# Kernel optimization log

Measured on AMD Instinct MI355X. Metric: run time of the kernel, lower is better.

The kernel has to match this reference:

```python
import jax, jax.numpy as jnp
import numpy as np

S, IN, OUT = 2048, 512, 512
H, KV = 16, 4            # query heads, kv heads (cross-broadcast + averaged)
DQ = DK = DV = 64        # per-head embedding dims


def setup_inputs() -> dict:
    key = jax.random.key(0)
    ks = jax.random.split(key, 5)
    lim_in = 1.0 / np.sqrt(IN)
    lim_o = 1.0 / np.sqrt(H * DV)
    x = jax.random.normal(ks[0], (S, IN), dtype=jnp.float32)
    Wq = jax.random.uniform(ks[1], (H * DQ, IN), jnp.float32, -lim_in, lim_in)
    Wk = jax.random.uniform(ks[2], (KV * DK, IN), jnp.float32, -lim_in, lim_in)
    Wv = jax.random.uniform(ks[3], (KV * DV, IN), jnp.float32, -lim_in, lim_in)
    Wo = jax.random.uniform(ks[4], (OUT, H * DV), jnp.float32, -lim_o, lim_o)
    return {"x": x, "Wq": Wq, "Wk": Wk, "Wv": Wv, "Wo": Wo}


def reference(x, Wq, Wk, Wv, Wo):
    seq = x.shape[0]
    # projections (eqx.nn.Linear: y = W @ x, no bias)
    q = (x @ Wq.T).reshape(seq, H, DQ)    # [S, H, DQ]
    k = (x @ Wk.T).reshape(seq, KV, DK)   # [S, KV, DK]
    v = (x @ Wv.T).reshape(seq, KV, DV)   # [S, KV, DV]
    # cross-broadcast every kv head against every query head -> [KV, H, S, S]
    scores = jnp.einsum('shd,tkd->khst', q, k) / jnp.sqrt(jnp.asarray(DK, x.dtype))
    # NOTE: original applies causal mask whenever `mask is not None`; the
    # boolean flag is always passed, so masking is effectively always on.
    causal = jnp.tril(jnp.ones((seq, seq), dtype=bool))
    scores = jnp.where(causal, scores, -jnp.inf)
    w = jax.nn.softmax(scores, axis=-1)   # [KV, H, S, S]
    # attn @ V, then sum over kv heads and average by KV
    o = jnp.einsum('khst,tkd->shd', w, v) / KV  # [S, H, DV]
    return o.reshape(seq, H * DV) @ Wo.T        # [S, OUT]
```

## Files before the change

### kernel.cpp

```cpp
#include <hip/hip_runtime.h>
#include <hip/hip_bf16.h>

#define SEQ   2048
#define INF_  512
#define HQ    16
#define KVH   4
#define DH    64
#define NQ    (HQ*DH)
#define NKV   (KVH*DH)
#define OUTD  512

typedef short v8s __attribute__((ext_vector_type(8)));
typedef float v4f __attribute__((ext_vector_type(4)));

static __device__ __forceinline__ float bf2f(unsigned short u) {
    union { unsigned int i; float f; } c;
    c.i = ((unsigned int)u) << 16;
    return c.f;
}
static __device__ __forceinline__ unsigned short f2bf(float f) {
    union { float f; unsigned int i; } c; c.f = f;
    unsigned int lsb = (c.i >> 16) & 1u;
    c.i += 0x7fffu + lsb;
    return (unsigned short)(c.i >> 16);
}
static __device__ __forceinline__ unsigned int f2bf2(float lo, float hi) {
    union { __hip_bfloat162 h; unsigned int u; } c;
    c.h = __float22bfloat162_rn(make_float2(lo, hi));
    return c.u;
}
static __device__ __forceinline__ v8s pack8(v4f a, v4f b) {
    union { v8s s; uint4 u; } c;
    c.u = make_uint4(f2bf2(a[0], a[1]), f2bf2(a[2], a[3]),
                     f2bf2(b[0], b[1]), f2bf2(b[2], b[3]));
    return c.s;
}

static __device__ __forceinline__ void gll16(const void* g, void* l) {
    __builtin_amdgcn_global_load_lds(
        (const __attribute__((address_space(1))) void*)g,
        (__attribute__((address_space(3))) void*)l, 16, 0, 0);
}

static __device__ __forceinline__ void stage_tile(
    const unsigned short* __restrict__ src, int stride, int kb,
    unsigned short* ldsbase, int w, int lane)
{
#pragma unroll
    for (int i = 0; i < 2; i++) {
        const int rl = w * 16 + i * 8 + (lane >> 3);
        const int kc = ((lane & 7) ^ (rl & 7)) * 8;
        gll16(src + (size_t)rl * stride + kb + kc,
              ldsbase + (w * 16 + i * 8) * 64);
    }
}

static __device__ __forceinline__ void stage_tile32(
    const unsigned short* __restrict__ src, int stride, int kb,
    unsigned short* ldsbase, int w, int lane)
{
    const int rl = w * 8 + (lane >> 3);
    const int kc = ((lane & 7) ^ (rl & 7)) * 8;
    gll16(src + (size_t)rl * stride + kb + kc,
          ldsbase + (w * 8) * 64);
}

#define QSCALE 0.180336880f

__global__ __launch_bounds__(256) void cast_all(
    const float* __restrict__ x,  const float* __restrict__ Wq,
    const float* __restrict__ Wk, const float* __restrict__ Wv,
    const float* __restrict__ Wo,
    unsigned short* __restrict__ xb,  unsigned short* __restrict__ Wqb,
    unsigned short* __restrict__ Wkb, unsigned short* __restrict__ Wvb,
    unsigned short* __restrict__ Wob)
{
    size_t i = ((size_t)blockIdx.x * 256 + threadIdx.x) * 8;
    const float* s; unsigned short* d; size_t off;
    if (i < 1048576)      { s = x;  d = xb;  off = i; }
    else if (i < 1572864) { s = Wq; d = Wqb; off = i - 1048576; }
    else if (i < 1703936) { s = Wk; d = Wkb; off = i - 1572864; }
    else if (i < 1835008) { s = Wv; d = Wvb; off = i - 1703936; }
    else                  { s = Wo; d = Wob; off = i - 1835008; }
    float4 a = *(const float4*)(s + off);
    float4 b = *(const float4*)(s + off + 4);
    *(uint4*)(d + off) = make_uint4(f2bf2(a.x, a.y), f2bf2(a.z, a.w),
                                    f2bf2(b.x, b.y), f2bf2(b.z, b.w));
}

__global__ __launch_bounds__(256, 4) void gemm_qkv(
    const unsigned short* __restrict__ xb,
    const unsigned short* __restrict__ Wqb,
    const unsigned short* __restrict__ Wkb,
    const unsigned short* __restrict__ Wvb,
    unsigned short* __restrict__ Qg,
    unsigned short* __restrict__ Kg,
    unsigned short* __restrict__ Vg)
{
    __shared__ unsigned short Asb[2][4096];
    __shared__ unsigned short Bsb[2][4096];

    const int m0 = blockIdx.x * 64;
    const int n0 = blockIdx.y * 64;

    const unsigned short* Bp; int role;
    if (n0 < NQ)            { Bp = Wqb + (size_t)n0 * INF_;              role = 0; }
    else if (n0 < NQ + NKV) { Bp = Wkb + (size_t)(n0 - NQ) * INF_;       role = 1; }
    else                    { Bp = Wvb + (size_t)(n0 - NQ - NKV) * INF_; role = 2; }

    const int tid = threadIdx.x;
    const int w = tid >> 6, lane = tid & 63;
    const int n = lane & 15, quad = lane >> 4;
    const int m7 = n & 7;
    const int r0w = (w & 1) * 32, c0w = (w >> 1) * 32;
    const unsigned short* Ap = xb + (size_t)m0 * INF_;

    v4f acc[2][2];
#pragma unroll
    for (int rt = 0; rt < 2; rt++)
#pragma unroll
        for (int ct = 0; ct < 2; ct++) acc[rt][ct] = (v4f){0.f,0.f,0.f,0.f};

    stage_tile(Ap, INF_, 0, &Asb[0][0], w, lane);
    stage_tile(Bp, INF_, 0, &Bsb[0][0], w, lane);

    for (int kb = 0; kb < INF_; kb += 64) {
        const int buf = (kb >> 6) & 1;
        __syncthreads();
        if (kb + 64 < INF_) {
            stage_tile(Ap, INF_, kb + 64, &Asb[buf ^ 1][0], w, lane);
            stage_tile(Bp, INF_, kb + 64, &Bsb[buf ^ 1][0], w, lane);
        }
#pragma unroll
        for (int kk = 0; kk < 2; kk++) {
            const int gs = ((kk * 4 + quad) ^ m7) * 8;
            v8s a0 = *(const v8s*)&Asb[buf][(r0w + n) * 64 + gs];
            v8s a1 = *(const v8s*)&Asb[buf][(r0w + 16 + n) * 64 + gs];
            v8s b0 = *(const v8s*)&Bsb[buf][(c0w + n) * 64 + gs];
            v8s b1 = *(const v8s*)&Bsb[buf][(c0w + 16 + n) * 64 + gs];
            acc[0][0] = __builtin_amdgcn_mfma_f32_16x16x32_bf16(a0, b0, acc[0][0], 0, 0, 0);
            acc[0][1] = __builtin_amdgcn_mfma_f32_16x16x32_bf16(a0, b1, acc[0][1], 0, 0, 0);
            acc[1][0] = __builtin_amdgcn_mfma_f32_16x16x32_bf16(a1, b0, acc[1][0], 0, 0, 0);
            acc[1][1] = __builtin_amdgcn_mfma_f32_16x16x32_bf16(a1, b1, acc[1][1], 0, 0, 0);
        }
    }

    const int t = m0 >> 6;
    if (role == 0) {
        unsigned short* base = Qg + ((size_t)(t * 16 + (n0 >> 6))) * 4096;
#pragma unroll
        for (int rt = 0; rt < 2; rt++)
#pragma unroll
            for (int ct = 0; ct < 2; ct++)
#pragma unroll
                for (int reg = 0; reg < 4; reg++) {
                    const int r = r0w + rt * 16 + quad * 4 + reg;
                    const int d = c0w + ct * 16 + n;
                    base[r * 64 + (((d >> 3) ^ (r & 7)) * 8) + (d & 7)] =
                        f2bf(acc[rt][ct][reg] * QSCALE);
                }
    } else if (role == 1) {
        const int g = (n0 - NQ) >> 6;
        unsigned short* base = Kg + ((size_t)(g * 32 + t)) * 4096;
#pragma unroll
        for (int rt = 0; rt < 2; rt++)
#pragma unroll
            for (int ct = 0; ct < 2; ct++)
#pragma unroll
                for (int reg = 0; reg < 4; reg++) {
                    const int r = r0w + rt * 16 + quad * 4 + reg;
                    const int d = c0w + ct * 16 + n;
                    base[r * 64 + (((d >> 3) ^ (r & 7)) * 8) + (d & 7)] =
                        f2bf(acc[rt][ct][reg]);
                }
    } else {
        const int g = (n0 - NQ - NKV) >> 6;
        unsigned short* base = Vg + ((size_t)(g * 32 + t)) * 4096;
#pragma unroll
        for (int rt = 0; rt < 2; rt++)
#pragma unroll
            for (int ct = 0; ct < 2; ct++) {
                const int jb_ = r0w + rt * 16 + quad * 4;
                const int d = c0w + ct * 16 + n;
                const int p = (jb_ & 32) + (((jb_ >> 2) & 3) * 8) + (((jb_ >> 4) & 1) * 4);
                *(uint2*)&base[d * 64 + (((p >> 3) ^ (d & 7)) * 8) + (p & 7)] =
                    make_uint2(f2bf2(acc[rt][ct][0], acc[rt][ct][1]),
                               f2bf2(acc[rt][ct][2], acc[rt][ct][3]));
            }
    }
}

__global__ __launch_bounds__(256, 2) void attn_mfma(
    const unsigned short* __restrict__ Qg,
    const unsigned short* __restrict__ Kg,
    const unsigned short* __restrict__ Vg,
    unsigned short* __restrict__ Oh)
{
    __shared__ unsigned short Ksb[2][4096];
    __shared__ unsigned short Vsb[2][4096];

    const int bx = blockIdx.x;
    const int hg = bx & 7;
    const int p  = (bx >> 3) & 7;
    const int sp = (bx >> 6) & 1;
    const int g  = bx >> 7;
    const int tid = threadIdx.x;
    const int w = tid >> 6, lane = tid & 63;
    const int n = lane & 15, quad = lane >> 4;
    const int m7 = n & 7;
    const int fo0 = (quad ^ m7) * 8;
    const int fo1 = ((quad + 4) ^ m7) * 8;

    v8s ones;
#pragma unroll
    for (int i = 0; i < 8; i++) ones[i] = (short)0x3F80;
    const v4f z = (v4f){0.f,0.f,0.f,0.f};

    unsigned short* Ohp = Oh + (size_t)g * ((size_t)SEQ * NQ);

    for (int half = 0; half < 2; half++) {
        const int qi2 = half ? (15 - p) : p;
        const int ext = 2 * qi2 + sp + 1;
        const int rowbase = qi2 * 128 + sp * 64 + w * 16;

        if (half) __syncthreads();

        {
            const size_t off = ((size_t)(g * 32)) * 4096 + w * 1024 + lane * 8;
            gll16(Kg + off,       &Ksb[0][w * 1024]);
            gll16(Kg + off + 512, &Ksb[0][w * 1024 + 512]);
            gll16(Vg + off,       &Vsb[0][w * 1024]);
            gll16(Vg + off + 512, &Vsb[0][w * 1024 + 512]);
        }

        v8s qa0, qa1, qb0, qb1;
        {
            const unsigned short* rpA =
                Qg + ((size_t)((2 * qi2 + sp) * 16 + hg * 2)) * 4096 + (w * 16 + n) * 64;
            const unsigned short* rpB = rpA + 4096;
            qa0 = *(const v8s*)(rpA + fo0);
            qa1 = *(const v8s*)(rpA + fo1);
            qb0 = *(const v8s*)(rpB + fo0);
            qb1 = *(const v8s*)(rpB + fo1);
        }

        v4f LA = (v4f){0.f,0.f,0.f,0.f};
        v4f LB = (v4f){0.f,0.f,0.f,0.f};
        v4f OA[4], OB[4];
#pragma unroll
        for (int dt = 0; dt < 4; dt++) { OA[dt] = z; OB[dt] = z; }

        for (int tt = 0; tt < ext; tt++) {
            const int buf = tt & 1;
            __syncthreads();
            if (tt + 1 < ext) {
                const size_t off = ((size_t)(g * 32 + tt + 1)) * 4096 + w * 1024 + lane * 8;
                const int nb = buf ^ 1;
                gll16(Kg + off,       &Ksb[nb][w * 1024]);
                gll16(Kg + off + 512, &Ksb[nb][w * 1024 + 512]);
                gll16(Vg + off,       &Vsb[nb][w * 1024]);
                gll16(Vg + off + 512, &Vsb[nb][w * 1024 + 512]);
            }
            const unsigned short* Kb = Ksb[buf];
            const unsigned short* Vb = Vsb[buf];

            v4f sa[4], sb[4];
            __builtin_amdgcn_s_setprio(1);
#pragma unroll
            for (int jt = 0; jt < 4; jt++) {
                const int kr = (jt * 16 + n) * 64;
                v8s k0 = *(const v8s*)&Kb[kr + fo0];
                v8s k1 = *(const v8s*)&Kb[kr + fo1];
                v4f ta = __builtin_amdgcn_mfma_f32_16x16x32_bf16(k0, qa0, z, 0, 0, 0);
                sa[jt] = __builtin_amdgcn_mfma_f32_16x16x32_bf16(k1, qa1, ta, 0, 0, 0);
                v4f tb = __builtin_amdgcn_mfma_f32_16x16x32_bf16(k0, qb0, z, 0, 0, 0);
                sb[jt] = __builtin_amdgcn_mfma_f32_16x16x32_bf16(k1, qb1, tb, 0, 0, 0);
            }
            __builtin_amdgcn_s_setprio(0);

            const int t0 = tt * 64;
            if (t0 + 63 > rowbase) {
                const int qg = rowbase + n;
#pragma unroll
                for (int jt = 0; jt < 4; jt++) {
                    const int jg = t0 + jt * 16 + quad * 4;
#pragma unroll
                    for (int reg = 0; reg < 4; reg++) {
                        const bool keep = (jg + reg <= qg);
                        sa[jt][reg] = keep ? sa[jt][reg] : -INFINITY;
                        sb[jt][reg] = keep ? sb[jt][reg] : -INFINITY;
                    }
                }
            }
#pragma unroll
            for (int jt = 0; jt < 4; jt++)
#pragma unroll
                for (int reg = 0; reg < 4; reg++) {
                    sa[jt][reg] = __builtin_amdgcn_exp2f(sa[jt][reg]);
                    sb[jt][reg] = __builtin_amdgcn_exp2f(sb[jt][reg]);
                }

            v8s pA0 = pack8(sa[0], sa[1]);
            v8s pA1 = pack8(sa[2], sa[3]);
            v8s pB0 = pack8(sb[0], sb[1]);
            v8s pB1 = pack8(sb[2], sb[3]);

            __builtin_amdgcn_s_setprio(1);
            LA = __builtin_amdgcn_mfma_f32_16x16x32_bf16(ones, pA0, LA, 0, 0, 0);
            LA = __builtin_amdgcn_mfma_f32_16x16x32_bf16(ones, pA1, LA, 0, 0, 0);
            LB = __builtin_amdgcn_mfma_f32_16x16x32_bf16(ones, pB0, LB, 0, 0, 0);
            LB = __builtin_amdgcn_mfma_f32_16x16x32_bf16(ones, pB1, LB, 0, 0, 0);

#pragma unroll
            for (int dt = 0; dt < 4; dt++) {
                const int vr = (dt * 16 + n) * 64;
                v8s v0 = *(const v8s*)&Vb[vr + fo0];
                v8s v1 = *(const v8s*)&Vb[vr + fo1];
                OA[dt] = __builtin_amdgcn_mfma_f32_16x16x32_bf16(v0, pA0, OA[dt], 0, 0, 0);
                OA[dt] = __builtin_amdgcn_mfma_f32_16x16x32_bf16(v1, pA1, OA[dt], 0, 0, 0);
                OB[dt] = __builtin_amdgcn_mfma_f32_16x16x32_bf16(v0, pB0, OB[dt], 0, 0, 0);
                OB[dt] = __builtin_amdgcn_mfma_f32_16x16x32_bf16(v1, pB1, OB[dt], 0, 0, 0);
            }
            __builtin_amdgcn_s_setprio(0);
        }

        {
            const float invA = 0.25f / LA[0];
            const float invB = 0.25f / LB[0];
            const int row = rowbase + n;
            unsigned short* dA = Ohp + (size_t)row * NQ + (hg * 2) * DH + quad * 4;
            unsigned short* dB = dA + DH;
#pragma unroll
            for (int dt = 0; dt < 4; dt++) {
                uint2 pkA = make_uint2(f2bf2(OA[dt][0] * invA, OA[dt][1] * invA),
                                       f2bf2(OA[dt][2] * invA, OA[dt][3] * invA));
                *(uint2*)(dA + dt * 16) = pkA;
                uint2 pkB = make_uint2(f2bf2(OB[dt][0] * invB, OB[dt][1] * invB),
                                       f2bf2(OB[dt][2] * invB, OB[dt][3] * invB));
                *(uint2*)(dB + dt * 16) = pkB;
            }
        }
    }
}

__global__ __launch_bounds__(256) void sum4(
    const unsigned short* __restrict__ Oh,
    unsigned short* __restrict__ Os)
{
    const size_t i = ((size_t)blockIdx.x * 256 + threadIdx.x) * 8;
    const size_t plane = (size_t)SEQ * NQ;
    uint4 u0 = *(const uint4*)(Oh + i);
    uint4 u1 = *(const uint4*)(Oh + plane + i);
    uint4 u2 = *(const uint4*)(Oh + 2 * plane + i);
    uint4 u3 = *(const uint4*)(Oh + 3 * plane + i);
    unsigned int ow[4];
#pragma unroll
    for (int q = 0; q < 4; q++) {
        const unsigned int a = ((const unsigned int*)&u0)[q];
        const unsigned int b = ((const unsigned int*)&u1)[q];
        const unsigned int c = ((const unsigned int*)&u2)[q];
        const unsigned int d = ((const unsigned int*)&u3)[q];
        float lo = bf2f((unsigned short)(a & 0xffffu)) + bf2f((unsigned short)(b & 0xffffu))
                 + bf2f((unsigned short)(c & 0xffffu)) + bf2f((unsigned short)(d & 0xffffu));
        float hi = bf2f((unsigned short)(a >> 16)) + bf2f((unsigned short)(b >> 16))
                 + bf2f((unsigned short)(c >> 16)) + bf2f((unsigned short)(d >> 16));
        ow[q] = f2bf2(lo, hi);
    }
    *(uint4*)(Os + i) = make_uint4(ow[0], ow[1], ow[2], ow[3]);
}

__global__ __launch_bounds__(256, 4) void gemm_out(
    const unsigned short* __restrict__ Os,
    const unsigned short* __restrict__ Wob,
    float* __restrict__ C)
{
    __shared__ unsigned short Asb[2][2048];
    __shared__ unsigned short Bsb[2][4096];

    const int m0 = blockIdx.x * 32;
    const int n0 = blockIdx.y * 64;
    const int tid = threadIdx.x;
    const int w = tid >> 6, lane = tid & 63;
    const int n = lane & 15, quad = lane >> 4;
    const int m7 = n & 7;
    const int rw = (w & 1) * 16, cw = (w >> 1) * 32;

    const unsigned short* Ap = Os + (size_t)m0 * NQ;
    const unsigned short* Bp = Wob + (size_t)n0 * NQ;

    v4f acc[2];
    acc[0] = (v4f){0.f,0.f,0.f,0.f};
    acc[1] = (v4f){0.f,0.f,0.f,0.f};

    stage_tile32(Ap, NQ, 0, &Asb[0][0], w, lane);
    stage_tile  (Bp, NQ, 0, &Bsb[0][0], w, lane);

    for (int kb = 0; kb < NQ; kb += 64) {
        const int buf = (kb >> 6) & 1;
        __syncthreads();
        if (kb + 64 < NQ) {
            stage_tile32(Ap, NQ, kb + 64, &Asb[buf ^ 1][0], w, lane);
            stage_tile  (Bp, NQ, kb + 64, &Bsb[buf ^ 1][0], w, lane);
        }
#pragma unroll
        for (int kk = 0; kk < 2; kk++) {
            const int gs = ((kk * 4 + quad) ^ m7) * 8;
            v8s a  = *(const v8s*)&Asb[buf][(rw + n) * 64 + gs];
            v8s b0 = *(const v8s*)&Bsb[buf][(cw + n) * 64 + gs];
            v8s b1 = *(const v8s*)&Bsb[buf][(cw + 16 + n) * 64 + gs];
            acc[0] = __builtin_amdgcn_mfma_f32_16x16x32_bf16(a, b0, acc[0], 0, 0, 0);
            acc[1] = __builtin_amdgcn_mfma_f32_16x16x32_bf16(a, b1, acc[1], 0, 0, 0);
        }
    }

#pragma unroll
    for (int ct = 0; ct < 2; ct++)
#pragma unroll
        for (int reg = 0; reg < 4; reg++) {
            const int row = m0 + rw + quad * 4 + reg;
            const int col = n0 + cw + ct * 16 + n;
            C[(size_t)row * OUTD + col] = acc[ct][reg];
        }
}

extern "C" void kernel_launch(void* const* d_in, const int* in_sizes, int n_in,
                              void* d_out, int out_size, void* d_ws, size_t ws_size,
                              hipStream_t stream) {
    const float* x  = (const float*)d_in[0];
    const float* Wq = (const float*)d_in[1];
    const float* Wk = (const float*)d_in[2];
    const float* Wv = (const float*)d_in[3];
    const float* Wo = (const float*)d_in[4];
    float* out = (float*)d_out;

    char* base = (char*)d_ws;
    unsigned short* Oh  = (unsigned short*)(base);
    unsigned short* xb  = (unsigned short*)(base);
    unsigned short* Wqb = (unsigned short*)(base + 2097152);
    unsigned short* Wkb = (unsigned short*)(base + 3145728);
    unsigned short* Wvb = (unsigned short*)(base + 3407872);
    unsigned short* Qg  = (unsigned short*)(base + 16777216);
    unsigned short* Kg  = (unsigned short*)(base + 20971520);
    unsigned short* Vg  = (unsigned short*)(base + 22020096);
    unsigned short* Wob = (unsigned short*)(base + 23068672);
    unsigned short* Os  = Qg;

    dim3 blk(256);
    cast_all<<<dim3(1152), blk, 0, stream>>>(x, Wq, Wk, Wv, Wo,
                                             xb, Wqb, Wkb, Wvb, Wob);
    gemm_qkv<<<dim3(SEQ / 64, (NQ + 2 * NKV) / 64), blk, 0, stream>>>(
        xb, Wqb, Wkb, Wvb, Qg, Kg, Vg);
    attn_mfma<<<dim3(512), blk, 0, stream>>>(Qg, Kg, Vg, Oh);
    sum4<<<dim3(1024), blk, 0, stream>>>(Oh, Os);
    gemm_out<<<dim3(SEQ / 32, OUTD / 64), blk, 0, stream>>>(Os, Wob, out);
}
```

Measured before the change: 139.3 us.

## Fuse fp32-to-bf16 casts into GEMMs and fold kv-head sum into output GEMM

Removes the standalone cast kernel by having the QKV and output GEMMs load fp32 inputs and weights directly and convert to bf16 while staging into LDS. Removes the sum4 kernel by having the output GEMM read the four per-kv-head partial outputs and sum them during its A-tile staging. This saves two launches plus the intermediate global round-trips. In exchange, staging now goes through registers with synchronous loads instead of async global_load_lds. The output GEMM drops from double- to single-buffered LDS with padded rows, and weights are recast on every block that reads them, which adds redundant conversion work.

New measurement: 139.5 us. Within noise of the previous version (+0.2%).

```diff
diff --git a/kernel.cpp b/kernel.cpp
--- a/kernel.cpp
+++ b/kernel.cpp
@@ -42,57 +42,30 @@
         (__attribute__((address_space(3))) void*)l, 16, 0, 0);
 }
 
-static __device__ __forceinline__ void stage_tile(
-    const unsigned short* __restrict__ src, int stride, int kb,
+static __device__ __forceinline__ void stage_tile_f32(
+    const float* __restrict__ src, int stride, int kb,
     unsigned short* ldsbase, int w, int lane)
 {
 #pragma unroll
     for (int i = 0; i < 2; i++) {
         const int rl = w * 16 + i * 8 + (lane >> 3);
         const int kc = ((lane & 7) ^ (rl & 7)) * 8;
-        gll16(src + (size_t)rl * stride + kb + kc,
-              ldsbase + (w * 16 + i * 8) * 64);
+        const float* sp = src + (size_t)rl * stride + kb + kc;
+        float4 a = *(const float4*)(sp);
+        float4 b = *(const float4*)(sp + 4);
+        *(uint4*)(ldsbase + (w * 16 + i * 8) * 64 + lane * 8) =
+            make_uint4(f2bf2(a.x, a.y), f2bf2(a.z, a.w),
+                       f2bf2(b.x, b.y), f2bf2(b.z, b.w));
     }
 }
 
-static __device__ __forceinline__ void stage_tile32(
-    const unsigned short* __restrict__ src, int stride, int kb,
-    unsigned short* ldsbase, int w, int lane)
-{
-    const int rl = w * 8 + (lane >> 3);
-    const int kc = ((lane & 7) ^ (rl & 7)) * 8;
-    gll16(src + (size_t)rl * stride + kb + kc,
-          ldsbase + (w * 8) * 64);
-}
-
 #define QSCALE 0.180336880f
 
-__global__ __launch_bounds__(256) void cast_all(
-    const float* __restrict__ x,  const float* __restrict__ Wq,
-    const float* __restrict__ Wk, const float* __restrict__ Wv,
-    const float* __restrict__ Wo,
-    unsigned short* __restrict__ xb,  unsigned short* __restrict__ Wqb,
-    unsigned short* __restrict__ Wkb, unsigned short* __restrict__ Wvb,
-    unsigned short* __restrict__ Wob)
-{
-    size_t i = ((size_t)blockIdx.x * 256 + threadIdx.x) * 8;
-    const float* s; unsigned short* d; size_t off;
-    if (i < 1048576)      { s = x;  d = xb;  off = i; }
-    else if (i < 1572864) { s = Wq; d = Wqb; off = i - 1048576; }
-    else if (i < 1703936) { s = Wk; d = Wkb; off = i - 1572864; }
-    else if (i < 1835008) { s = Wv; d = Wvb; off = i - 1703936; }
-    else                  { s = Wo; d = Wob; off = i - 1835008; }
-    float4 a = *(const float4*)(s + off);
-    float4 b = *(const float4*)(s + off + 4);
-    *(uint4*)(d + off) = make_uint4(f2bf2(a.x, a.y), f2bf2(a.z, a.w),
-                                    f2bf2(b.x, b.y), f2bf2(b.z, b.w));
-}
-
 __global__ __launch_bounds__(256, 4) void gemm_qkv(
-    const unsigned short* __restrict__ xb,
-    const unsigned short* __restrict__ Wqb,
-    const unsigned short* __restrict__ Wkb,
-    const unsigned short* __restrict__ Wvb,
+    const float* __restrict__ x,
+    const float* __restrict__ Wq,
+    const float* __restrict__ Wk,
+    const float* __restrict__ Wv,
     unsigned short* __restrict__ Qg,
     unsigned short* __restrict__ Kg,
     unsigned short* __restrict__ Vg)
@@ -103,17 +76,17 @@
     const int m0 = blockIdx.x * 64;
     const int n0 = blockIdx.y * 64;
 
-    const unsigned short* Bp; int role;
-    if (n0 < NQ)            { Bp = Wqb + (size_t)n0 * INF_;              role = 0; }
-    else if (n0 < NQ + NKV) { Bp = Wkb + (size_t)(n0 - NQ) * INF_;       role = 1; }
-    else                    { Bp = Wvb + (size_t)(n0 - NQ - NKV) * INF_; role = 2; }
+    const float* Bp; int role;
+    if (n0 < NQ)            { Bp = Wq + (size_t)n0 * INF_;              role = 0; }
+    else if (n0 < NQ + NKV) { Bp = Wk + (size_t)(n0 - NQ) * INF_;       role = 1; }
+    else                    { Bp = Wv + (size_t)(n0 - NQ - NKV) * INF_; role = 2; }
 
     const int tid = threadIdx.x;
     const int w = tid >> 6, lane = tid & 63;
     const int n = lane & 15, quad = lane >> 4;
     const int m7 = n & 7;
     const int r0w = (w & 1) * 32, c0w = (w >> 1) * 32;
-    const unsigned short* Ap = xb + (size_t)m0 * INF_;
+    const float* Ap = x + (size_t)m0 * INF_;
 
     v4f acc[2][2];
 #pragma unroll
@@ -121,15 +94,15 @@
 #pragma unroll
         for (int ct = 0; ct < 2; ct++) acc[rt][ct] = (v4f){0.f,0.f,0.f,0.f};
 
-    stage_tile(Ap, INF_, 0, &Asb[0][0], w, lane);
-    stage_tile(Bp, INF_, 0, &Bsb[0][0], w, lane);
+    stage_tile_f32(Ap, INF_, 0, &Asb[0][0], w, lane);
+    stage_tile_f32(Bp, INF_, 0, &Bsb[0][0], w, lane);
 
     for (int kb = 0; kb < INF_; kb += 64) {
         const int buf = (kb >> 6) & 1;
         __syncthreads();
         if (kb + 64 < INF_) {
-            stage_tile(Ap, INF_, kb + 64, &Asb[buf ^ 1][0], w, lane);
-            stage_tile(Bp, INF_, kb + 64, &Bsb[buf ^ 1][0], w, lane);
+            stage_tile_f32(Ap, INF_, kb + 64, &Asb[buf ^ 1][0], w, lane);
+            stage_tile_f32(Bp, INF_, kb + 64, &Bsb[buf ^ 1][0], w, lane);
         }
 #pragma unroll
         for (int kk = 0; kk < 2; kk++) {
@@ -343,71 +316,76 @@
     }
 }
 
-__global__ __launch_bounds__(256) void sum4(
+__global__ __launch_bounds__(256, 4) void gemm_out(
     const unsigned short* __restrict__ Oh,
-    unsigned short* __restrict__ Os)
-{
-    const size_t i = ((size_t)blockIdx.x * 256 + threadIdx.x) * 8;
-    const size_t plane = (size_t)SEQ * NQ;
-    uint4 u0 = *(const uint4*)(Oh + i);
-    uint4 u1 = *(const uint4*)(Oh + plane + i);
-    uint4 u2 = *(const uint4*)(Oh + 2 * plane + i);
-    uint4 u3 = *(const uint4*)(Oh + 3 * plane + i);
-    unsigned int ow[4];
-#pragma unroll
-    for (int q = 0; q < 4; q++) {
-        const unsigned int a = ((const unsigned int*)&u0)[q];
-        const unsigned int b = ((const unsigned int*)&u1)[q];
-        const unsigned int c = ((const unsigned int*)&u2)[q];
-        const unsigned int d = ((const unsigned int*)&u3)[q];
-        float lo = bf2f((unsigned short)(a & 0xffffu)) + bf2f((unsigned short)(b & 0xffffu))
-                 + bf2f((unsigned short)(c & 0xffffu)) + bf2f((unsigned short)(d & 0xffffu));
-        float hi = bf2f((unsigned short)(a >> 16)) + bf2f((unsigned short)(b >> 16))
-                 + bf2f((unsigned short)(c >> 16)) + bf2f((unsigned short)(d >> 16));
-        ow[q] = f2bf2(lo, hi);
-    }
-    *(uint4*)(Os + i) = make_uint4(ow[0], ow[1], ow[2], ow[3]);
-}
-
-__global__ __launch_bounds__(256, 4) void gemm_out(
-    const unsigned short* __restrict__ Os,
-    const unsigned short* __restrict__ Wob,
+    const float* __restrict__ Wo,
     float* __restrict__ C)
 {
-    __shared__ unsigned short Asb[2][2048];
-    __shared__ unsigned short Bsb[2][4096];
+    __shared__ unsigned short Asb[32][72];
+    __shared__ unsigned short Bsb[64][72];
 
     const int m0 = blockIdx.x * 32;
     const int n0 = blockIdx.y * 64;
     const int tid = threadIdx.x;
     const int w = tid >> 6, lane = tid & 63;
     const int n = lane & 15, quad = lane >> 4;
-    const int m7 = n & 7;
     const int rw = (w & 1) * 16, cw = (w >> 1) * 32;
-
-    const unsigned short* Ap = Os + (size_t)m0 * NQ;
-    const unsigned short* Bp = Wob + (size_t)n0 * NQ;
+    const int ar = tid >> 3, akc = (tid & 7) * 8;
+    const int br = tid >> 2, bkc = (tid & 3) * 16;
 
     v4f acc[2];
     acc[0] = (v4f){0.f,0.f,0.f,0.f};
     acc[1] = (v4f){0.f,0.f,0.f,0.f};
 
-    stage_tile32(Ap, NQ, 0, &Asb[0][0], w, lane);
-    stage_tile  (Bp, NQ, 0, &Bsb[0][0], w, lane);
+    const size_t plane = (size_t)SEQ * NQ;
+    const size_t abase = (size_t)(m0 + ar) * NQ + akc;
+    const float* bp = Wo + (size_t)(n0 + br) * NQ + bkc;
+
+    uint4 ua[4];
+#pragma unroll
+    for (int g = 0; g < 4; g++) ua[g] = *(const uint4*)(Oh + g * plane + abase);
+    float4 ub0 = *(const float4*)(bp),      ub1 = *(const float4*)(bp + 4);
+    float4 ub2 = *(const float4*)(bp + 8),  ub3 = *(const float4*)(bp + 12);
 
     for (int kb = 0; kb < NQ; kb += 64) {
-        const int buf = (kb >> 6) & 1;
+        __syncthreads();
+        {
+            unsigned int ow[4];
+#pragma unroll
+            for (int q = 0; q < 4; q++) {
+                const unsigned int u0 = ((const unsigned int*)&ua[0])[q];
+                const unsigned int u1 = ((const unsigned int*)&ua[1])[q];
+                const unsigned int u2 = ((const unsigned int*)&ua[2])[q];
+                const unsigned int u3 = ((const unsigned int*)&ua[3])[q];
+                float lo = bf2f((unsigned short)(u0 & 0xffffu)) + bf2f((unsigned short)(u1 & 0xffffu))
+                         + bf2f((unsigned short)(u2 & 0xffffu)) + bf2f((unsigned short)(u3 & 0xffffu));
+                float hi = bf2f((unsigned short)(u0 >> 16)) + bf2f((unsigned short)(u1 >> 16))
+                         + bf2f((unsigned short)(u2 >> 16)) + bf2f((unsigned short)(u3 >> 16));
+                ow[q] = f2bf2(lo, hi);
+            }
+            *(uint4*)&Asb[ar][akc] = make_uint4(ow[0], ow[1], ow[2], ow[3]);
+        }
+        *(uint4*)&Bsb[br][bkc] =
+            make_uint4(f2bf2(ub0.x, ub0.y), f2bf2(ub0.z, ub0.w),
+                       f2bf2(ub1.x, ub1.y), f2bf2(ub1.z, ub1.w));
+        *(uint4*)&Bsb[br][bkc + 8] =
+            make_uint4(f2bf2(ub2.x, ub2.y), f2bf2(ub2.z, ub2.w),
+                       f2bf2(ub3.x, ub3.y), f2bf2(ub3.z, ub3.w));
         __syncthreads();
         if (kb + 64 < NQ) {
-            stage_tile32(Ap, NQ, kb + 64, &Asb[buf ^ 1][0], w, lane);
-            stage_tile  (Bp, NQ, kb + 64, &Bsb[buf ^ 1][0], w, lane);
+#pragma unroll
+            for (int g = 0; g < 4; g++)
+                ua[g] = *(const uint4*)(Oh + g * plane + abase + kb + 64);
+            ub0 = *(const float4*)(bp + kb + 64);
+            ub1 = *(const float4*)(bp + kb + 64 + 4);
+            ub2 = *(const float4*)(bp + kb + 64 + 8);
+            ub3 = *(const float4*)(bp + kb + 64 + 12);
         }
 #pragma unroll
         for (int kk = 0; kk < 2; kk++) {
-            const int gs = ((kk * 4 + quad) ^ m7) * 8;
-            v8s a  = *(const v8s*)&Asb[buf][(rw + n) * 64 + gs];
-            v8s b0 = *(const v8s*)&Bsb[buf][(cw + n) * 64 + gs];
-            v8s b1 = *(const v8s*)&Bsb[buf][(cw + 16 + n) * 64 + gs];
+            v8s a  = *(const v8s*)&Asb[rw + n][kk * 32 + quad * 8];
+            v8s b0 = *(const v8s*)&Bsb[cw + n][kk * 32 + quad * 8];
+            v8s b1 = *(const v8s*)&Bsb[cw + 16 + n][kk * 32 + quad * 8];
             acc[0] = __builtin_amdgcn_mfma_f32_16x16x32_bf16(a, b0, acc[0], 0, 0, 0);
             acc[1] = __builtin_amdgcn_mfma_f32_16x16x32_bf16(a, b1, acc[1], 0, 0, 0);
         }
@@ -435,22 +413,13 @@
 
     char* base = (char*)d_ws;
     unsigned short* Oh  = (unsigned short*)(base);
-    unsigned short* xb  = (unsigned short*)(base);
-    unsigned short* Wqb = (unsigned short*)(base + 2097152);
-    unsigned short* Wkb = (unsigned short*)(base + 3145728);
-    unsigned short* Wvb = (unsigned short*)(base + 3407872);
     unsigned short* Qg  = (unsigned short*)(base + 16777216);
     unsigned short* Kg  = (unsigned short*)(base + 20971520);
     unsigned short* Vg  = (unsigned short*)(base + 22020096);
-    unsigned short* Wob = (unsigned short*)(base + 23068672);
-    unsigned short* Os  = Qg;
 
     dim3 blk(256);
-    cast_all<<<dim3(1152), blk, 0, stream>>>(x, Wq, Wk, Wv, Wo,
-                                             xb, Wqb, Wkb, Wvb, Wob);
     gemm_qkv<<<dim3(SEQ / 64, (NQ + 2 * NKV) / 64), blk, 0, stream>>>(
-        xb, Wqb, Wkb, Wvb, Qg, Kg, Vg);
+        x, Wq, Wk, Wv, Qg, Kg, Vg);
     attn_mfma<<<dim3(512), blk, 0, stream>>>(Qg, Kg, Vg, Oh);
-    sum4<<<dim3(1024), blk, 0, stream>>>(Oh, Os);
-    gemm_out<<<dim3(SEQ / 32, OUTD / 64), blk, 0, stream>>>(Os, Wob, out);
-}
+    gemm_out<<<dim3(SEQ / 32, OUTD / 64), blk, 0, stream>>>(Oh, Wo, out);
+}
```
